# Kernel tuning notes

Measured on AMD Instinct MI355X. Metric: run time of the kernel, lower is better.

## Reference

```python
import jax, jax.numpy as jnp
import numpy as np

NBATCH, NELEC, NATOMS, NBAS, NORB = 1024, 64, 16, 256, 128

# per-atom shell pattern: (l, m) pairs; bas_n = l (standard for GTO primitives)
_SHELL_LM = [(0, 0), (1, -1), (1, 0), (1, 1), (2, -2), (2, -1), (2, 0), (2, 1), (2, 2),
             (0, 0), (1, -1), (1, 0), (1, 1), (2, 0), (2, 2), (2, -2)]


def _norm_gaussian(bas_exp, bas_n):
    # Torch _norm_gaussian: bas_n += 1; A = exp**(0.25*(2n+1)); B = 2**(2n+1.5);
    # C = factorial2(2n-1)*sqrt(pi); norm = sqrt(B/C)*A
    n1 = bas_n + 1.0
    A = bas_exp ** (0.25 * (2.0 * n1 + 1.0))
    B = 2.0 ** (2.0 * n1 + 1.5)
    # 2*n1-1 in {1,3,5} for n in {0,1,2}: factorial2 -> {1,3,15}
    f2 = np.array([1.0, 3.0, 15.0], dtype=np.float32)[bas_n.astype(np.int32)]
    C = f2 * np.float32(np.sqrt(np.pi))
    return (np.sqrt(B / C) * A).astype(np.float32)


def setup_inputs() -> dict:
    key = jax.random.key(0)
    k0, k1, k2, k3, k4 = jax.random.split(key, 5)
    inp = jax.random.normal(k0, (NBATCH, NELEC, 3), jnp.float32) * 2.0
    atom_coords = jax.random.normal(k1, (NATOMS, 3), jnp.float32) * 3.0
    bas_exp = jax.random.uniform(k2, (NBAS,), jnp.float32, minval=0.2, maxval=3.0)
    bas_coeffs = jax.random.uniform(k3, (NBAS,), jnp.float32, minval=0.5, maxval=1.0)

    lm = np.array(_SHELL_LM * (NBAS // len(_SHELL_LM)), dtype=np.int32)  # [NBAS,2]
    bas_l = jnp.asarray(lm[:, 0])
    bas_m = jnp.asarray(lm[:, 1])
    bas_n = jnp.asarray(lm[:, 0].astype(np.float32))
    bas_atom_index = jnp.asarray((np.arange(NBAS) // (NBAS // NATOMS)).astype(np.int32))
    index_ctr = jnp.sort(jax.random.randint(k4, (NBAS,), 0, NORB)).astype(jnp.int32)
    norm_cst = jnp.asarray(_norm_gaussian(np.asarray(bas_exp), np.asarray(bas_n)))
    return {
        'input': inp, 'atom_coords': atom_coords, 'bas_exp': bas_exp,
        'bas_coeffs': bas_coeffs, 'norm_cst': norm_cst, 'bas_n': bas_n,
        'bas_l': bas_l, 'bas_m': bas_m, 'bas_atom_index': bas_atom_index,
        'index_ctr': index_ctr,
    }


def _spherical_harmonics(xyz, r, r2, bas_l, bas_m):
    # real spherical harmonics up to l=2 (QMCTorch constants)
    x, y, z = xyz[..., 0], xyz[..., 1], xyz[..., 2]
    C0 = 0.2820948          # 1/(2 sqrt(pi))
    C1 = 0.4886025          # sqrt(3/(4 pi))
    C2XY = 1.0925484        # sqrt(15/(4 pi))
    C2Z2 = 0.31539156       # sqrt(5/(16 pi))
    C2D = 0.5462742         # sqrt(15/(16 pi))
    y1 = C1 * jnp.where(bas_m == -1, y, jnp.where(bas_m == 0, z, x)) / r
    y2 = jnp.where(bas_m == -2, C2XY * x * y,
         jnp.where(bas_m == -1, C2XY * y * z,
         jnp.where(bas_m == 0, C2Z2 * (2.0 * z * z - x * x - y * y),
         jnp.where(bas_m == 1, C2XY * z * x, C2D * (x * x - y * y))))) / r2
    return jnp.where(bas_l == 0, C0, jnp.where(bas_l == 1, y1, y2))


def reference(input, atom_coords, bas_exp, bas_coeffs, norm_cst, bas_n,
              bas_l, bas_m, bas_atom_index, index_ctr):
    # bas_coords = atom_coords.repeat_interleave(nshells) expressed as a gather
    bas_coords = atom_coords[bas_atom_index]                     # [nbas, 3]
    xyz = input[:, :, None, :] - bas_coords[None, None, :, :]    # [B, E, nbas, 3]
    r2 = jnp.sum(xyz * xyz, axis=-1)                             # [B, E, nbas]
    r = jnp.sqrt(r2)
    R = r ** bas_n * jnp.exp(-bas_exp * r2)                      # gaussian radial
    Y = _spherical_harmonics(xyz, r, r2, bas_l, bas_m)
    bas = norm_cst * bas_coeffs * R * Y                          # [B, E, nbas]
    ao = jnp.zeros((input.shape[0], input.shape[1], NORB), bas.dtype)
    return ao.at[:, :, index_ctr].add(bas)                       # index_add over dim 2
```

## Files before the change

### kernel.cpp

```cpp
#include <hip/hip_runtime.h>

#define NBAS   256
#define NORB   128
#define NROWS  65536
#define RPB    16
#define NATOM  16
#define TSTR   12

__device__ __forceinline__ float wave_scan_incl(float x) {
    int t;
    t = __builtin_amdgcn_update_dpp(0, __float_as_int(x), 0x111, 0xf, 0xf, false);
    x += __int_as_float(t);
    t = __builtin_amdgcn_update_dpp(0, __float_as_int(x), 0x112, 0xf, 0xf, false);
    x += __int_as_float(t);
    t = __builtin_amdgcn_update_dpp(0, __float_as_int(x), 0x114, 0xf, 0xf, false);
    x += __int_as_float(t);
    t = __builtin_amdgcn_update_dpp(0, __float_as_int(x), 0x118, 0xf, 0xf, false);
    x += __int_as_float(t);
    t = __builtin_amdgcn_update_dpp(0, __float_as_int(x), 0x142, 0xa, 0xf, false);
    x += __int_as_float(t);
    t = __builtin_amdgcn_update_dpp(0, __float_as_int(x), 0x143, 0xc, 0xf, false);
    x += __int_as_float(t);
    return x;
}

__global__ __launch_bounds__(256, 5) void ao_kernel(
    const float* __restrict__ inp,
    const float* __restrict__ atom_coords,
    const float* __restrict__ bas_exp,
    const float* __restrict__ bas_coeffs,
    const float* __restrict__ norm_cst,
    const int*   __restrict__ bas_l,
    const int*   __restrict__ bas_m,
    const int*   __restrict__ bas_atom_index,
    const int*   __restrict__ index_ctr,
    float* __restrict__ out)
{
    __shared__ __align__(16) float s_tab[RPB][NATOM][TSTR];
    __shared__ __align__(16) float s_vals[RPB][NBAS];
    __shared__ int s_start[NORB + 1];

    const int tid  = threadIdx.x;
    const int row0 = blockIdx.x * RPB;

    const float nex = -bas_exp[tid] * 1.4426950408889634f;
    const int l = bas_l[tid], m = bas_m[tid];
    const float C0 = 0.2820948f, C1 = 0.4886025f, C2XY = 1.0925484f,
                C2Z2 = 0.31539156f, C2D = 0.5462742f;
    int idx; float C;
    if (l == 0)      { idx = 0; C = C0; }
    else if (l == 1) { idx = (m == -1) ? 2 : (m == 0) ? 3 : 1; C = C1; }
    else {
        if      (m == -2) { idx = 4; C = C2XY; }
        else if (m == -1) { idx = 5; C = C2XY; }
        else if (m ==  0) { idx = 6; C = C2Z2; }
        else if (m ==  1) { idx = 7; C = C2XY; }
        else              { idx = 8; C = C2D;  }
    }
    const float lcc = __log2f(norm_cst[tid] * bas_coeffs[tid] * C);
    const int atom = tid >> 4;
    const float* tmono = &s_tab[0][atom][0] + idx;
    const float* tr2   = &s_tab[0][atom][9];

    {
        int ic   = index_ctr[tid];
        int prev = (tid == 0) ? -1 : index_ctr[tid - 1];
        for (int o = prev + 1; o <= ic; ++o) s_start[o] = tid;
        if (tid == NBAS - 1)
            for (int o = ic + 1; o <= NORB; ++o) s_start[o] = NBAS;
    }

    {
        const int a = tid & 15, r = tid >> 4;
        float px = inp[(row0 + r)*3 + 0];
        float py = inp[(row0 + r)*3 + 1];
        float pz = inp[(row0 + r)*3 + 2];
        float x = px - atom_coords[a*3+0];
        float y = py - atom_coords[a*3+1];
        float z = pz - atom_coords[a*3+2];
        float x2 = x*x, y2 = y*y, z2 = z*z;
        float r2 = x2 + y2 + z2;
        float* e = &s_tab[r][a][0];
        reinterpret_cast<float4*>(e)[0] = make_float4(1.0f, x, y, z);
        reinterpret_cast<float4*>(e)[1] = make_float4(x*y, y*z, fmaf(3.f, z2, -r2), z*x);
        reinterpret_cast<float4*>(e)[2] = make_float4(x2 - y2, r2, 0.f, 0.f);
    }
    __syncthreads();

    #pragma unroll
    for (int r = 0; r < RPB; ++r) {
        float mono = tmono[r * NATOM * TSTR];
        float r2   = tr2  [r * NATOM * TSTR];
        float E = __builtin_exp2f(fmaf(nex, r2, lcc));
        s_vals[r][tid] = E * mono;
    }
    __syncthreads();

    const int w = tid >> 6, ln = tid & 63;
    #pragma unroll
    for (int r = 0; r < 4; ++r) {
        const int row = 4*w + r;
        float4 v = *reinterpret_cast<const float4*>(&s_vals[row][ln << 2]);
        float e0 = v.x;
        float e1 = e0 + v.y;
        float e2 = e1 + v.z;
        float e3 = e2 + v.w;
        float s    = wave_scan_incl(e3);
        float excl = s - e3;
        *reinterpret_cast<float4*>(&s_vals[row][ln << 2]) =
            make_float4(e0 + excl, e1 + excl, e2 + excl, e3 + excl);
    }

    #pragma unroll
    for (int g = 0; g < 2; ++g) {
        const int row = 4*w + 2*g + (ln >> 5);
        const int q   = (ln & 31) << 2;
        int st[5];
        #pragma unroll
        for (int k = 0; k < 5; ++k) st[k] = s_start[q + k];
        float p[5];
        #pragma unroll
        for (int k = 0; k < 5; ++k) {
            int i2 = st[k] - 1;
            float v = s_vals[row][i2 < 0 ? 0 : i2];
            p[k] = (st[k] > 0) ? v : 0.0f;
        }
        float4 o4 = make_float4(p[1]-p[0], p[2]-p[1], p[3]-p[2], p[4]-p[3]);
        *reinterpret_cast<float4*>(&out[(size_t)(row0 + row) * NORB + q]) = o4;
    }
}

extern "C" void kernel_launch(void* const* d_in, const int* in_sizes, int n_in,
                              void* d_out, int out_size, void* d_ws, size_t ws_size,
                              hipStream_t stream) {
    const float* inp   = (const float*)d_in[0];
    const float* atomc = (const float*)d_in[1];
    const float* bexp  = (const float*)d_in[2];
    const float* bcoef = (const float*)d_in[3];
    const float* bnorm = (const float*)d_in[4];
    const int* bl   = (const int*)d_in[6];
    const int* bm   = (const int*)d_in[7];
    const int* bai  = (const int*)d_in[8];
    const int* ictr = (const int*)d_in[9];
    float* out = (float*)d_out;

    hipLaunchKernelGGL(ao_kernel, dim3(NROWS / RPB), dim3(256), 0, stream,
                       inp, atomc, bexp, bcoef, bnorm, bl, bm, bai, ictr, out);
}
```

Baseline: 20.29 us.

## Make each wavefront own two rows and drop block-wide barriers

Rows per block drop from 16 to 8. Each 64-lane wavefront now handles its own two rows: it builds a private monomial table, its own copy of the start indices, evaluates four basis functions per lane, and does the prefix-sum scan and gather on its own. This removes both __syncthreads barriers and the shared staging of all basis values across the block. It relies on wave-synchronous LDS visibility between lanes without explicit barriers, and it redoes the per-basis parameter setup and start-table construction once per wave instead of once per block.

```diff
diff --git a/kernel.cpp b/kernel.cpp
--- a/kernel.cpp
+++ b/kernel.cpp
@@ -3,7 +3,7 @@
 #define NBAS   256
 #define NORB   128
 #define NROWS  65536
-#define RPB    16
+#define RPB    8
 #define NATOM  16
 #define TSTR   12
 
@@ -24,7 +24,7 @@
     return x;
 }
 
-__global__ __launch_bounds__(256, 5) void ao_kernel(
+__global__ __launch_bounds__(256, 8) void ao_kernel(
     const float* __restrict__ inp,
     const float* __restrict__ atom_coords,
     const float* __restrict__ bas_exp,
@@ -36,97 +36,111 @@
     const int*   __restrict__ index_ctr,
     float* __restrict__ out)
 {
-    __shared__ __align__(16) float s_tab[RPB][NATOM][TSTR];
-    __shared__ __align__(16) float s_vals[RPB][NBAS];
-    __shared__ int s_start[NORB + 1];
+    __shared__ __align__(16) float s_tab [4][2][NATOM][TSTR];
+    __shared__ __align__(16) float s_pref[4][2][NBAS];
+    __shared__ int s_start[4][NORB + 1];
 
-    const int tid  = threadIdx.x;
-    const int row0 = blockIdx.x * RPB;
+    const int tid = threadIdx.x;
+    const int w   = tid >> 6, ln = tid & 63;
+    const int rowbase = (int)blockIdx.x * RPB + 2 * w;
+    const int b4 = ln << 2;
 
-    const float nex = -bas_exp[tid] * 1.4426950408889634f;
-    const int l = bas_l[tid], m = bas_m[tid];
+    const float4 vex = *reinterpret_cast<const float4*>(&bas_exp[b4]);
+    const float4 vcf = *reinterpret_cast<const float4*>(&bas_coeffs[b4]);
+    const float4 vnm = *reinterpret_cast<const float4*>(&norm_cst[b4]);
+    const int4   vl  = *reinterpret_cast<const int4*>(&bas_l[b4]);
+    const int4   vm  = *reinterpret_cast<const int4*>(&bas_m[b4]);
+    const float exs[4] = {vex.x, vex.y, vex.z, vex.w};
+    const float cfs[4] = {vcf.x*vnm.x, vcf.y*vnm.y, vcf.z*vnm.z, vcf.w*vnm.w};
+    const int   ls[4]  = {vl.x, vl.y, vl.z, vl.w};
+    const int   ms[4]  = {vm.x, vm.y, vm.z, vm.w};
+
     const float C0 = 0.2820948f, C1 = 0.4886025f, C2XY = 1.0925484f,
                 C2Z2 = 0.31539156f, C2D = 0.5462742f;
-    int idx; float C;
-    if (l == 0)      { idx = 0; C = C0; }
-    else if (l == 1) { idx = (m == -1) ? 2 : (m == 0) ? 3 : 1; C = C1; }
-    else {
-        if      (m == -2) { idx = 4; C = C2XY; }
-        else if (m == -1) { idx = 5; C = C2XY; }
-        else if (m ==  0) { idx = 6; C = C2Z2; }
-        else if (m ==  1) { idx = 7; C = C2XY; }
-        else              { idx = 8; C = C2D;  }
+    float nex[4], lcc[4];
+    int   moff[4];
+    const int a4 = ln >> 2;
+    #pragma unroll
+    for (int k = 0; k < 4; ++k) {
+        int l = ls[k], m = ms[k], idx; float C;
+        if (l == 0)      { idx = 0; C = C0; }
+        else if (l == 1) { idx = (m == -1) ? 2 : (m == 0) ? 3 : 1; C = C1; }
+        else {
+            if      (m == -2) { idx = 4; C = C2XY; }
+            else if (m == -1) { idx = 5; C = C2XY; }
+            else if (m ==  0) { idx = 6; C = C2Z2; }
+            else if (m ==  1) { idx = 7; C = C2XY; }
+            else              { idx = 8; C = C2D;  }
+        }
+        nex[k]  = -exs[k] * 1.4426950408889634f;
+        lcc[k]  = __log2f(cfs[k] * C);
+        moff[k] = a4 * TSTR + idx;
     }
-    const float lcc = __log2f(norm_cst[tid] * bas_coeffs[tid] * C);
-    const int atom = tid >> 4;
-    const float* tmono = &s_tab[0][atom][0] + idx;
-    const float* tr2   = &s_tab[0][atom][9];
+    const int r2off = a4 * TSTR + 9;
 
+    int* sst = s_start[w];
     {
-        int ic   = index_ctr[tid];
-        int prev = (tid == 0) ? -1 : index_ctr[tid - 1];
-        for (int o = prev + 1; o <= ic; ++o) s_start[o] = tid;
-        if (tid == NBAS - 1)
-            for (int o = ic + 1; o <= NORB; ++o) s_start[o] = NBAS;
+        const int4 vic = *reinterpret_cast<const int4*>(&index_ctr[b4]);
+        const int ics[4] = {vic.x, vic.y, vic.z, vic.w};
+        int prev = (ln == 0) ? -1 : index_ctr[b4 - 1];
+        #pragma unroll
+        for (int k = 0; k < 4; ++k) {
+            for (int o = prev + 1; o <= ics[k]; ++o) sst[o] = b4 + k;
+            prev = ics[k];
+        }
+        if (ln == 63)
+            for (int o = ics[3] + 1; o <= NORB; ++o) sst[o] = NBAS;
     }
 
-    {
-        const int a = tid & 15, r = tid >> 4;
-        float px = inp[(row0 + r)*3 + 0];
-        float py = inp[(row0 + r)*3 + 1];
-        float pz = inp[(row0 + r)*3 + 2];
+    if (ln < 32) {
+        const int a = ln & 15, r = ln >> 4;
+        const int row = rowbase + r;
+        float px = inp[row*3+0], py = inp[row*3+1], pz = inp[row*3+2];
         float x = px - atom_coords[a*3+0];
         float y = py - atom_coords[a*3+1];
         float z = pz - atom_coords[a*3+2];
         float x2 = x*x, y2 = y*y, z2 = z*z;
         float r2 = x2 + y2 + z2;
-        float* e = &s_tab[r][a][0];
+        float* e = &s_tab[w][r][a][0];
         reinterpret_cast<float4*>(e)[0] = make_float4(1.0f, x, y, z);
         reinterpret_cast<float4*>(e)[1] = make_float4(x*y, y*z, fmaf(3.f, z2, -r2), z*x);
         reinterpret_cast<float4*>(e)[2] = make_float4(x2 - y2, r2, 0.f, 0.f);
     }
-    __syncthreads();
 
     #pragma unroll
-    for (int r = 0; r < RPB; ++r) {
-        float mono = tmono[r * NATOM * TSTR];
-        float r2   = tr2  [r * NATOM * TSTR];
-        float E = __builtin_exp2f(fmaf(nex, r2, lcc));
-        s_vals[r][tid] = E * mono;
-    }
-    __syncthreads();
-
-    const int w = tid >> 6, ln = tid & 63;
-    #pragma unroll
-    for (int r = 0; r < 4; ++r) {
-        const int row = 4*w + r;
-        float4 v = *reinterpret_cast<const float4*>(&s_vals[row][ln << 2]);
-        float e0 = v.x;
-        float e1 = e0 + v.y;
-        float e2 = e1 + v.z;
-        float e3 = e2 + v.w;
+    for (int r = 0; r < 2; ++r) {
+        const float* tb = &s_tab[w][r][0][0];
+        float r2 = tb[r2off];
+        float ev[4];
+        #pragma unroll
+        for (int k = 0; k < 4; ++k)
+            ev[k] = __builtin_exp2f(fmaf(nex[k], r2, lcc[k])) * tb[moff[k]];
+        float e0 = ev[0];
+        float e1 = e0 + ev[1];
+        float e2 = e1 + ev[2];
+        float e3 = e2 + ev[3];
         float s    = wave_scan_incl(e3);
         float excl = s - e3;
-        *reinterpret_cast<float4*>(&s_vals[row][ln << 2]) =
+        *reinterpret_cast<float4*>(&s_pref[w][r][b4]) =
             make_float4(e0 + excl, e1 + excl, e2 + excl, e3 + excl);
     }
 
-    #pragma unroll
-    for (int g = 0; g < 2; ++g) {
-        const int row = 4*w + 2*g + (ln >> 5);
-        const int q   = (ln & 31) << 2;
+    {
+        const int rr = ln >> 5;
+        const int q4 = (ln & 31) << 2;
+        const float* pf = s_pref[w][rr];
         int st[5];
         #pragma unroll
-        for (int k = 0; k < 5; ++k) st[k] = s_start[q + k];
+        for (int k = 0; k < 5; ++k) st[k] = sst[q4 + k];
         float p[5];
         #pragma unroll
         for (int k = 0; k < 5; ++k) {
             int i2 = st[k] - 1;
-            float v = s_vals[row][i2 < 0 ? 0 : i2];
+            float v = pf[i2 < 0 ? 0 : i2];
             p[k] = (st[k] > 0) ? v : 0.0f;
         }
         float4 o4 = make_float4(p[1]-p[0], p[2]-p[1], p[3]-p[2], p[4]-p[3]);
-        *reinterpret_cast<float4*>(&out[(size_t)(row0 + row) * NORB + q]) = o4;
+        *reinterpret_cast<float4*>(&out[(size_t)(rowbase + rr) * NORB + q4]) = o4;
     }
 }
 
```

Result: slower. 29.18 us (+43.8%).
